# Optimization experiments

Hardware: AMD Instinct MI355X
Metric: run time of the kernel (lower is better)

Reference implementation:

```python
import jax, jax.numpy as jnp
import numpy as np

NEG_INF = -1e12  # matches masked_fill value -1000000000000.0
LEAKY_SLOPE = 0.2


def setup_inputs() -> dict:
    key = jax.random.key(0)
    k1, k2, k3, k4, k5 = jax.random.split(key, 5)
    B, C, H, N, F_IN, F_OUT = 4, 4, 4, 1024, 64, 64
    h = jax.random.normal(k1, (B, C, N, F_IN), dtype=jnp.float32)
    adj = jax.random.randint(k2, (B, N, N), 0, 2).astype(jnp.float32)
    w = jax.random.normal(k3, (C, H, F_IN, F_OUT), dtype=jnp.float32) * 0.1
    a_src = jax.random.normal(k4, (C, H, F_OUT, 1), dtype=jnp.float32) * 0.1
    a_dst = jax.random.normal(k5, (C, H, F_OUT, 1), dtype=jnp.float32) * 0.1
    return {"h": h, "adj": adj, "w": w, "a_src": a_src, "a_dst": a_dst}


def reference(h, adj, w, a_src, a_dst):
    # h: [B,C,N,f_in], w: [C,H,f_in,f_out] -> h_prime: [B,C,H,N,f_out]
    h_prime = jnp.einsum('bcnf,chfo->bchno', h, w)
    t = jnp.tanh(h_prime)
    # additive attention scores: [B,C,H,N]
    attn_src = jnp.einsum('bchno,cho->bchn', t, a_src[..., 0])
    attn_dst = jnp.einsum('bchno,cho->bchn', t, a_dst[..., 0])
    # attn[b,c,h,i,j] = src[i] + dst[j]  -> [B,C,H,N,N]
    attn = attn_src[..., :, None] + attn_dst[..., None, :]
    attn = jnp.where(attn >= 0, attn, LEAKY_SLOPE * attn)  # leaky_relu(0.2)
    N = h.shape[2]
    adj_sl = adj + jnp.eye(N, dtype=adj.dtype)  # add self-loops
    mask = (adj_sl == 0)[:, None, None, :, :]   # [B,1,1,N,N]
    attn = jnp.where(mask, NEG_INF, attn)
    attn = jax.nn.softmax(attn, axis=-1)
    # dropout is identity (attn_dropout=0.0 / eval mode)
    out = jnp.einsum('bchnm,bchmo->bchno', attn, h_prime)
    return out
```

## Files before the change

kernel.cpp:

```cpp
#include <hip/hip_runtime.h>
#include <hip/hip_bf16.h>
#include <math.h>

#define NB 4
#define NC 4
#define NH 4
#define NN 1024
#define NF 64
#define NCOMBO 64
#define LEAK 0.2f

typedef __attribute__((ext_vector_type(8)))  short  short8;
typedef __attribute__((ext_vector_type(16))) float  float16;

static __device__ __forceinline__ unsigned pk_bf16(float a, float b) {
    union { __hip_bfloat162 h; unsigned u; } cv;
    cv.h = __float22bfloat162_rn(make_float2(a, b));
    return cv.u;
}

static __device__ __forceinline__ float fast_tanh(float x) {
    const float e = __expf(2.f * x);
    return 1.f - 2.f * __builtin_amdgcn_rcpf(1.f + e);
}

static __device__ __forceinline__ void async_cp16(const void* gsrc, void* ldst) {
    __builtin_amdgcn_global_load_lds(
        (const __attribute__((address_space(1))) unsigned int*)gsrc,
        (__attribute__((address_space(3))) unsigned int*)ldst, 16, 0, 0);
}

static __device__ __forceinline__ void split8(const float4 a, const float4 b,
                                              short8* hi, short8* lo) {
    union { short8 v; unsigned u[4]; } H, L;
    const float x[8] = {a.x,a.y,a.z,a.w,b.x,b.y,b.z,b.w};
    float lov[8];
    #pragma unroll
    for (int p = 0; p < 4; ++p) {
        const unsigned pk = pk_bf16(x[2*p], x[2*p+1]);
        H.u[p] = pk;
        union { unsigned u; float f; } f0, f1;
        f0.u = pk << 16; f1.u = pk & 0xffff0000u;
        lov[2*p]   = x[2*p]   - f0.f;
        lov[2*p+1] = x[2*p+1] - f1.f;
    }
    #pragma unroll
    for (int p = 0; p < 4; ++p) L.u[p] = pk_bf16(lov[2*p], lov[2*p+1]);
    *hi = H.v; *lo = L.v;
}

__global__ __launch_bounds__(256) void gA_produce(
    const float* __restrict__ h, const float* __restrict__ adj,
    const float* __restrict__ w, const float* __restrict__ a_src,
    const float* __restrict__ a_dst,
    unsigned short* __restrict__ hpt, float* __restrict__ asrc,
    unsigned* __restrict__ tblG, unsigned long long* __restrict__ bits)
{
    __shared__ __align__(16) char smem[17920];
    float* w_s    = (float*)smem;
    unsigned short* whi = (unsigned short*)smem;
    unsigned short* wlo = (unsigned short*)(smem + 8192);
    float* as_lds = (float*)(smem + 16384);
    float* ad_lds = (float*)(smem + 16640);
    float* scS    = (float*)(smem + 16896);
    float* scD    = (float*)(smem + 17408);

    const int idx  = blockIdx.x;
    const int t    = threadIdx.x;
    const int g    = (idx & 7)*8 + ((idx >> 3) & 7);
    const int tile = idx >> 6;
    const int b = g >> 4, c = (g >> 2) & 3, hh = g & 3;
    const int lane = t & 63, l31 = lane & 31, half = lane >> 5;
    const int wv = t >> 6, rg = wv >> 1, oh = wv & 1;

    const float4* wsrc = (const float4*)(w + ((size_t)(c*NH + hh))*NF*NF);
    #pragma unroll
    for (int i = 0; i < 4; ++i)
        ((float4*)w_s)[t + i*256] = wsrc[t + i*256];
    if (t < NF) {
        as_lds[t] = a_src[(c*NH + hh)*NF + t];
        ad_lds[t] = a_dst[(c*NH + hh)*NF + t];
    }
    __syncthreads();

    float wv0[8], wv1[8];
    {
        const int n = t & 31;
        #pragma unroll
        for (int j = 0; j < 8; ++j) {
            const int blk0 = t >> 5, blk1 = (t >> 5) + 8;
            const int k0 = (blk0 >> 2)*16 + (blk0 & 1)*8 + j;
            const int o0 = ((blk0 >> 1) & 1)*32 + n;
            const int k1 = (blk1 >> 2)*16 + (blk1 & 1)*8 + j;
            const int o1 = ((blk1 >> 1) & 1)*32 + n;
            wv0[j] = w_s[k0*64 + o0];
            wv1[j] = w_s[k1*64 + o1];
        }
    }
    short8 ahi[4], alo[4];
    {
        const float* hrow = h +
            (((size_t)(b*NC + c))*NN + tile*64 + rg*32 + l31)*NF;
        #pragma unroll
        for (int s = 0; s < 4; ++s) {
            const float4 v0 = *(const float4*)&hrow[s*16 + half*8];
            const float4 v1 = *(const float4*)&hrow[s*16 + half*8 + 4];
            split8(v0, v1, &ahi[s], &alo[s]);
        }
    }
    __syncthreads();

    {
        union { short8 v; unsigned u[4]; } H; short8 L;
        float4 a0 = make_float4(wv0[0],wv0[1],wv0[2],wv0[3]);
        float4 a1 = make_float4(wv0[4],wv0[5],wv0[6],wv0[7]);
        split8(a0, a1, &H.v, &L);
        *(short8*)&whi[((t >> 5)*32 + (t & 31))*8] = H.v;
        *(short8*)&wlo[((t >> 5)*32 + (t & 31))*8] = L;
        a0 = make_float4(wv1[0],wv1[1],wv1[2],wv1[3]);
        a1 = make_float4(wv1[4],wv1[5],wv1[6],wv1[7]);
        split8(a0, a1, &H.v, &L);
        *(short8*)&whi[(((t >> 5) + 8)*32 + (t & 31))*8] = H.v;
        *(short8*)&wlo[(((t >> 5) + 8)*32 + (t & 31))*8] = L;
    }
    __syncthreads();

    float16 acc;
    #pragma unroll
    for (int i = 0; i < 16; ++i) acc[i] = 0.f;
    #pragma unroll
    for (int s = 0; s < 4; ++s) {
        const short8 bhi = *(const short8*)&whi[(((s*2 + oh)*2 + half)*32 + l31)*8];
        const short8 blo = *(const short8*)&wlo[(((s*2 + oh)*2 + half)*32 + l31)*8];
        acc = __builtin_amdgcn_mfma_f32_32x32x16_bf16(ahi[s], bhi, acc, 0, 0, 0);
        acc = __builtin_amdgcn_mfma_f32_32x32x16_bf16(alo[s], bhi, acc, 0, 0, 0);
        acc = __builtin_amdgcn_mfma_f32_32x32x16_bf16(ahi[s], blo, acc, 0, 0, 0);
    }

    {
        const int col = oh*32 + l31;
        const float av = as_lds[col], dv = ad_lds[col];
        float sS[16], sD[16];
        #pragma unroll
        for (int reg = 0; reg < 16; ++reg) {
            const float tt = fast_tanh(acc[reg]);
            sS[reg] = tt * av;
            sD[reg] = tt * dv;
        }
        #pragma unroll
        for (int off = 1; off <= 16; off <<= 1) {
            #pragma unroll
            for (int reg = 0; reg < 16; ++reg) {
                sS[reg] += __shfl_xor(sS[reg], off);
                sD[reg] += __shfl_xor(sD[reg], off);
            }
        }
        if (l31 == 0) {
            #pragma unroll
            for (int reg = 0; reg < 16; ++reg) {
                const int row = rg*32 + (reg & 3) + 8*(reg >> 2) + 4*half;
                scS[row*2 + oh] = sS[reg];
                scD[row*2 + oh] = sD[reg];
            }
        }
    }

    {
        unsigned short* dst = hpt + ((size_t)(g*16 + tile))*4096;
        #pragma unroll
        for (int q = 0; q < 4; ++q) {
            const int ks = rg*2 + (q >> 1), hf = q & 1;
            const int elem = (((ks*2 + oh)*2 + hf)*32 + l31)*8 + 4*half;
            uint2 pk;
            pk.x = pk_bf16(acc[q*4 + 0], acc[q*4 + 1]);
            pk.y = pk_bf16(acc[q*4 + 2], acc[q*4 + 3]);
            *(uint2*)&dst[elem] = pk;
        }
    }
    __syncthreads();
    if (t < 64) {
        const float s = scS[t*2] + scS[t*2 + 1];
        const float d = scD[t*2] + scD[t*2 + 1];
        asrc[(size_t)g*NN + tile*64 + t] = s;
        tblG[(size_t)g*NN + tile*64 + t] = pk_bf16(__expf(LEAK*d), __expf(d));
    }

    {
        const int base = idx*4096;
        #pragma unroll
        for (int q = 0; q < 16; ++q) {
            const int e  = base + q*256 + t;
            const int j  = e & (NN-1);
            const int i  = (e >> 10) & (NN-1);
            const int bb = e >> 20;
            const bool pred = (adj[e] != 0.f) || (j == i);
            const unsigned long long m = __ballot(pred);
            if ((t & 63) == 0) bits[((size_t)bb*NN + i)*16 + (j >> 6)] = m;
        }
    }
}

__global__ __launch_bounds__(256, 4) void gC_attn(
    const unsigned short* __restrict__ hpt, const float* __restrict__ asrc,
    const unsigned* __restrict__ tblG,
    const unsigned long long* __restrict__ bits, float* __restrict__ out)
{
    __shared__ __align__(16) char smem[25600];
    unsigned short* fragB = (unsigned short*)smem;
    float*          comb  = (float*)smem;
    unsigned long long* bits_lds = (unsigned long long*)(smem + 16384);
    float*          psum2 = (float*)(smem + 17408);

    const int idx = blockIdx.x;
    const int t   = threadIdx.x;
    const int g   = (idx & 7)*8 + ((idx >> 3) & 7);
    const int it  = idx >> 6;
    const int b   = g >> 4;
    const int i0  = it*64;
    const int wv = t >> 6, lane = t & 63;
    const int l31 = lane & 31, half = lane >> 5;
    const int rg = wv >> 1, jh = wv & 1;
    const int myrow = rg*32 + l31;

    {
        const char* gs = (const char*)hpt + ((size_t)g*16)*8192 + wv*2048 + lane*16;
        char* ls = smem + wv*2048;
        async_cp16(gs, ls);
        async_cp16(gs + 1024, ls + 1024);
    }
    {
        const unsigned long long* bsrc = bits + ((size_t)b*NN + i0)*16;
        #pragma unroll
        for (int q = 0; q < 4; ++q) {
            const int e = q*256 + t;
            bits_lds[(e >> 4)*17 + (e & 15)] = bsrc[e];
        }
    }
    const float sv    = asrc[(size_t)g*NN + i0 + myrow];
    const float ratio = __expf((LEAK - 1.f)*sv);
    const unsigned* tb = tblG + (size_t)g*NN;

    union { short8 v; unsigned short u[8]; } ONES;
    #pragma unroll
    for (int i = 0; i < 8; ++i) ONES.u[i] = 0x3F80;

    float16 acc0, acc1, acc2;
    #pragma unroll
    for (int i = 0; i < 16; ++i) { acc0[i] = 0.f; acc1[i] = 0.f; acc2[i] = 0.f; }

    for (int jt = 0; jt < 16; ++jt) {
        __syncthreads();
        const int fb = jt & 1;
        if (jt < 15) {
            const char* gs = (const char*)hpt + ((size_t)g*16 + jt + 1)*8192
                             + wv*2048 + lane*16;
            char* ls = smem + ((jt + 1) & 1)*8192 + wv*2048;
            async_cp16(gs, ls);
            async_cp16(gs + 1024, ls + 1024);
        }
        const unsigned long long wb = bits_lds[myrow*17 + jt];

        #pragma unroll
        for (int kk = 0; kk < 2; ++kk) {
            const int ks = jh*2 + kk;
            const int jo = ks*16 + half*8;
            const uint4 Ta = *(const uint4*)&tb[jt*64 + jo];
            const uint4 Tb = *(const uint4*)&tb[jt*64 + jo + 4];
            const short8 b0 = *(const short8*)
                &fragB[fb*4096 + (((ks*2 + 0)*2 + half)*32 + l31)*8];
            const short8 b1 = *(const short8*)
                &fragB[fb*4096 + (((ks*2 + 1)*2 + half)*32 + l31)*8];
            const unsigned bb = (unsigned)(wb >> jo) & 0xffu;

            float p0, p1, p2, p3, p4, p5, p6, p7;
            {
                union { unsigned u; float f; } hi, lo;
                hi.u = Ta.x & 0xffff0000u; lo.u = Ta.x << 16;
                p0 = fmaxf(hi.f, ratio*lo.f); p0 = (bb & 1u)   ? p0 : 0.f;
                hi.u = Ta.y & 0xffff0000u; lo.u = Ta.y << 16;
                p1 = fmaxf(hi.f, ratio*lo.f); p1 = (bb & 2u)   ? p1 : 0.f;
                hi.u = Ta.z & 0xffff0000u; lo.u = Ta.z << 16;
                p2 = fmaxf(hi.f, ratio*lo.f); p2 = (bb & 4u)   ? p2 : 0.f;
                hi.u = Ta.w & 0xffff0000u; lo.u = Ta.w << 16;
                p3 = fmaxf(hi.f, ratio*lo.f); p3 = (bb & 8u)   ? p3 : 0.f;
                hi.u = Tb.x & 0xffff0000u; lo.u = Tb.x << 16;
                p4 = fmaxf(hi.f, ratio*lo.f); p4 = (bb & 16u)  ? p4 : 0.f;
                hi.u = Tb.y & 0xffff0000u; lo.u = Tb.y << 16;
                p5 = fmaxf(hi.f, ratio*lo.f); p5 = (bb & 32u)  ? p5 : 0.f;
                hi.u = Tb.z & 0xffff0000u; lo.u = Tb.z << 16;
                p6 = fmaxf(hi.f, ratio*lo.f); p6 = (bb & 64u)  ? p6 : 0.f;
                hi.u = Tb.w & 0xffff0000u; lo.u = Tb.w << 16;
                p7 = fmaxf(hi.f, ratio*lo.f); p7 = (bb & 128u) ? p7 : 0.f;
            }

            union { short8 v; unsigned u[4]; } af;
            af.u[0] = pk_bf16(p0, p1);
            af.u[1] = pk_bf16(p2, p3);
            af.u[2] = pk_bf16(p4, p5);
            af.u[3] = pk_bf16(p6, p7);

            acc2 = __builtin_amdgcn_mfma_f32_32x32x16_bf16(af.v, ONES.v, acc2, 0, 0, 0);
            acc0 = __builtin_amdgcn_mfma_f32_32x32x16_bf16(af.v, b0,     acc0, 0, 0, 0);
            acc1 = __builtin_amdgcn_mfma_f32_32x32x16_bf16(af.v, b1,     acc1, 0, 0, 0);
        }
    }

    __syncthreads();

    if (l31 == 0) {
        #pragma unroll
        for (int reg = 0; reg < 16; ++reg) {
            const int r = (reg & 3) + 8*(reg >> 2) + 4*half;
            psum2[jh*64 + rg*32 + r] = acc2[reg];
        }
    }
    if (jh == 1) {
        float* cb = comb + (rg*64 + lane)*34;
        #pragma unroll
        for (int i = 0; i < 8; ++i) {
            float2 v0; v0.x = acc0[2*i]; v0.y = acc0[2*i+1];
            float2 v1; v1.x = acc1[2*i]; v1.y = acc1[2*i+1];
            *(float2*)&cb[2*i]      = v0;
            *(float2*)&cb[16 + 2*i] = v1;
        }
    }
    __syncthreads();
    if (jh == 0) {
        const float* cb = comb + (rg*64 + lane)*34;
        #pragma unroll
        for (int i = 0; i < 8; ++i) {
            const float2 v0 = *(const float2*)&cb[2*i];
            const float2 v1 = *(const float2*)&cb[16 + 2*i];
            acc0[2*i] += v0.x; acc0[2*i+1] += v0.y;
            acc1[2*i] += v1.x; acc1[2*i+1] += v1.y;
        }
        #pragma unroll
        for (int reg = 0; reg < 16; ++reg) {
            const int r = (reg & 3) + 8*(reg >> 2) + 4*half;
            const int row = rg*32 + r;
            const float inv = __builtin_amdgcn_rcpf(psum2[row] + psum2[64 + row]);
            const size_t base = ((size_t)g*NN + i0 + row)*NF;
            out[base + l31]      = acc0[reg] * inv;
            out[base + l31 + 32] = acc1[reg] * inv;
        }
    }
}

extern "C" void kernel_launch(void* const* d_in, const int* in_sizes, int n_in,
                              void* d_out, int out_size, void* d_ws, size_t ws_size,
                              hipStream_t stream)
{
    const float* h     = (const float*)d_in[0];
    const float* adj   = (const float*)d_in[1];
    const float* w     = (const float*)d_in[2];
    const float* a_src = (const float*)d_in[3];
    const float* a_dst = (const float*)d_in[4];
    float* out = (float*)d_out;

    char* ws = (char*)d_ws;
    unsigned short* hpt = (unsigned short*)ws;
    float* asrc         = (float*)(ws + 8388608);
    unsigned* tblG      = (unsigned*)(ws + 8388608 + 262144);
    unsigned long long* bits = (unsigned long long*)(ws + 8388608 + 524288);

    gA_produce<<<dim3(1024), dim3(256), 0, stream>>>(
        h, adj, w, a_src, a_dst, hpt, asrc, tblG, bits);
    gC_attn<<<dim3(1024), dim3(256), 0, stream>>>(
        hpt, asrc, tblG, bits, out);
}
```

Before: 120.8 us.

## Use per-wave triple-buffered async loads and drop per-tile block barriers

Replaces the block-wide double-buffered LDS staging of h' fragments with a per-wave three-slot ring. Each wave loads only the fragments it consumes, two steps ahead, and synchronises with explicit vmcnt/lgkmcnt waits instead of a __syncthreads per j-tile. It also stages the per-graph score table into LDS once up front instead of reading it from global memory in the loop. The aim is to remove barrier stalls and hide global latency, at the cost of more LDS (lower occupancy risk) and correctness relying on hand-written waitcnt counts.

```diff
diff --git a/kernel.cpp b/kernel.cpp
--- a/kernel.cpp
+++ b/kernel.cpp
@@ -28,6 +28,14 @@
     __builtin_amdgcn_global_load_lds(
         (const __attribute__((address_space(1))) unsigned int*)gsrc,
         (__attribute__((address_space(3))) unsigned int*)ldst, 16, 0, 0);
+}
+
+static __device__ __forceinline__ void wait_vm4()  { asm volatile("s_waitcnt vmcnt(4)"   ::: "memory"); }
+static __device__ __forceinline__ void wait_vm2()  { asm volatile("s_waitcnt vmcnt(2)"   ::: "memory"); }
+static __device__ __forceinline__ void wait_vm0()  { asm volatile("s_waitcnt vmcnt(0)"   ::: "memory"); }
+static __device__ __forceinline__ void wait_lgkm0(){ asm volatile("s_waitcnt lgkmcnt(0)" ::: "memory"); }
+static __device__ __forceinline__ void wait_vm(int s) {
+    if (s < 30) wait_vm4(); else if (s == 30) wait_vm2(); else wait_vm0();
 }
 
 static __device__ __forceinline__ void split8(const float4 a, const float4 b,
@@ -205,11 +213,11 @@
     const unsigned* __restrict__ tblG,
     const unsigned long long* __restrict__ bits, float* __restrict__ out)
 {
-    __shared__ __align__(16) char smem[25600];
-    unsigned short* fragB = (unsigned short*)smem;
+    __shared__ __align__(16) char smem[37376];
+    unsigned*       tbl   = (unsigned*)(smem + 24576);
+    unsigned long long* bits_lds = (unsigned long long*)(smem + 28672);
     float*          comb  = (float*)smem;
-    unsigned long long* bits_lds = (unsigned long long*)(smem + 16384);
-    float*          psum2 = (float*)(smem + 17408);
+    float*          psum2 = (float*)(smem + 28672);
 
     const int idx = blockIdx.x;
     const int t   = threadIdx.x;
@@ -222,11 +230,18 @@
     const int rg = wv >> 1, jh = wv & 1;
     const int myrow = rg*32 + l31;
 
-    {
-        const char* gs = (const char*)hpt + ((size_t)g*16)*8192 + wv*2048 + lane*16;
-        char* ls = smem + wv*2048;
-        async_cp16(gs, ls);
-        async_cp16(gs + 1024, ls + 1024);
+    const char* hbase = (const char*)hpt + ((size_t)g*16)*8192 + jh*4096 + lane*16;
+    char* ring = smem + wv*6144;
+
+    async_cp16(hbase,        ring);
+    async_cp16(hbase + 1024, ring + 1024);
+    async_cp16(hbase + 2048, ring + 2048);
+    async_cp16(hbase + 3072, ring + 3072);
+
+    #pragma unroll
+    for (int q = 0; q < 4; ++q) {
+        const int j = q*256 + t;
+        tbl[j] = tblG[(size_t)g*NN + j];
     }
     {
         const unsigned long long* bsrc = bits + ((size_t)b*NN + i0)*16;
@@ -238,7 +253,6 @@
     }
     const float sv    = asrc[(size_t)g*NN + i0 + myrow];
     const float ratio = __expf((LEAK - 1.f)*sv);
-    const unsigned* tb = tblG + (size_t)g*NN;
 
     union { short8 v; unsigned short u[8]; } ONES;
     #pragma unroll
@@ -248,28 +262,32 @@
     #pragma unroll
     for (int i = 0; i < 16; ++i) { acc0[i] = 0.f; acc1[i] = 0.f; acc2[i] = 0.f; }
 
+    __syncthreads();
+
+    #pragma unroll
     for (int jt = 0; jt < 16; ++jt) {
-        __syncthreads();
-        const int fb = jt & 1;
-        if (jt < 15) {
-            const char* gs = (const char*)hpt + ((size_t)g*16 + jt + 1)*8192
-                             + wv*2048 + lane*16;
-            char* ls = smem + ((jt + 1) & 1)*8192 + wv*2048;
-            async_cp16(gs, ls);
-            async_cp16(gs + 1024, ls + 1024);
-        }
         const unsigned long long wb = bits_lds[myrow*17 + jt];
 
         #pragma unroll
         for (int kk = 0; kk < 2; ++kk) {
+            const int s = jt*2 + kk;
+            if (s < 30) {
+                wait_lgkm0();
+                const int t2 = s + 2;
+                const char* gs = hbase + (size_t)(t2 >> 1)*8192 + (t2 & 1)*2048;
+                char* ls = ring + (t2 % 3)*2048;
+                async_cp16(gs, ls);
+                async_cp16(gs + 1024, ls + 1024);
+            }
+            wait_vm(s);
+
             const int ks = jh*2 + kk;
             const int jo = ks*16 + half*8;
-            const uint4 Ta = *(const uint4*)&tb[jt*64 + jo];
-            const uint4 Tb = *(const uint4*)&tb[jt*64 + jo + 4];
-            const short8 b0 = *(const short8*)
-                &fragB[fb*4096 + (((ks*2 + 0)*2 + half)*32 + l31)*8];
-            const short8 b1 = *(const short8*)
-                &fragB[fb*4096 + (((ks*2 + 1)*2 + half)*32 + l31)*8];
+            const uint4 Ta = *(const uint4*)&tbl[jt*64 + jo];
+            const uint4 Tb = *(const uint4*)&tbl[jt*64 + jo + 4];
+            const char* sb = ring + (s % 3)*2048;
+            const short8 b0 = *(const short8*)(sb + half*512 + l31*16);
+            const short8 b1 = *(const short8*)(sb + 1024 + half*512 + l31*16);
             const unsigned bb = (unsigned)(wb >> jo) & 0xffu;
 
             float p0, p1, p2, p3, p4, p5, p6, p7;
```

After: 119.5 us. No clear change (-1.0%).
